# Optimization experiments

Measured on AMD Instinct MI355X. Metric: run time of the kernel, lower is better.

The kernel has to match this reference:

```python
import jax, jax.numpy as jnp
import numpy as np

B, T, C, H = 4, 2048, 768, 12
D = C // H
EPS = 1e-5


def layernorm(x, g, b):
    mu = jnp.mean(x, axis=-1, keepdims=True)
    var = jnp.mean(jnp.square(x - mu), axis=-1, keepdims=True)
    return (x - mu) * jax.lax.rsqrt(var + EPS) * g + b


def setup_inputs() -> dict:
    key = jax.random.key(0)
    ks = jax.random.split(key, 16)
    s = 0.02
    return {
        "x": jax.random.normal(ks[0], (B, T, C), jnp.float32),
        "Wq": jax.random.normal(ks[1], (C, C), jnp.float32) * s,
        "bq": jnp.zeros((C,), jnp.float32),
        "Wk": jax.random.normal(ks[2], (C, C), jnp.float32) * s,
        "bk": jnp.zeros((C,), jnp.float32),
        "Wv": jax.random.normal(ks[3], (C, C), jnp.float32) * s,
        "bv": jnp.zeros((C,), jnp.float32),
        "Wo": jax.random.normal(ks[4], (C, C), jnp.float32) * s,
        "bo": jnp.zeros((C,), jnp.float32),
        "g1": jnp.ones((C,), jnp.float32),
        "b1": jnp.zeros((C,), jnp.float32),
        "g2": jnp.ones((C,), jnp.float32),
        "b2": jnp.zeros((C,), jnp.float32),
        "W1": jax.random.normal(ks[5], (C, 4 * C), jnp.float32) * s,
        "bm1": jnp.zeros((4 * C,), jnp.float32),
        "W2": jax.random.normal(ks[6], (4 * C, C), jnp.float32) * s,
        "bm2": jnp.zeros((C,), jnp.float32),
    }


def reference(x, Wq, bq, Wk, bk, Wv, bv, Wo, bo, g1, b1, g2, b2, W1, bm1, W2, bm2):
    # --- attention branch ---
    h = layernorm(x, g1, b1)
    q = (h @ Wq + bq).reshape(B, T, H, D)
    k = (h @ Wk + bk).reshape(B, T, H, D)
    v = (h @ Wv + bv).reshape(B, T, H, D)
    att = jnp.einsum('bqhd,bkhd->bhqk', q, k) / jnp.sqrt(jnp.float32(D))
    causal = jnp.tril(jnp.ones((T, T), bool))
    att = jnp.where(causal, att, -jnp.inf)
    att = jax.nn.softmax(att, axis=-1)
    o = jnp.einsum('bhqk,bkhd->bqhd', att, v).reshape(B, T, C)
    x = x + o @ Wo + bo
    # --- MLP branch ---
    h = layernorm(x, g2, b2)
    h = jax.nn.gelu(h @ W1 + bm1, approximate=False)
    return x + h @ W2 + bm2
```

## Files before the change

### kernel.cpp

```cpp
#include <hip/hip_runtime.h>
#include <hip/hip_bf16.h>

#define B_ 4
#define T_ 2048
#define C_ 768
#define H_ 12
#define D_ 64
#define QS_ 2304

typedef __attribute__((ext_vector_type(8))) short short8;
typedef __attribute__((ext_vector_type(4))) short short4v;
typedef __attribute__((ext_vector_type(4))) float f32x4;

__device__ __forceinline__ unsigned short f2bf(float f) {
    __hip_bfloat16 h = __float2bfloat16(f);
    return *reinterpret_cast<unsigned short*>(&h);
}

__device__ __forceinline__ unsigned cvt_pk_bf16(float lo, float hi) {
    unsigned r;
    asm("v_cvt_pk_bf16_f32 %0, %1, %2" : "=v"(r) : "v"(lo), "v"(hi));
    return r;
}

__device__ __forceinline__ void gl_lds16(const void* g, void* l) {
    __builtin_amdgcn_global_load_lds((const __attribute__((address_space(1))) unsigned int*)g,
                                     (__attribute__((address_space(3))) unsigned int*)l,
                                     16, 0, 0);
}

__device__ __forceinline__ void transpose_dev(const float* __restrict__ W,
                                              unsigned short* __restrict__ Wt,
                                              int K, int N, int bx, int by,
                                              float (*t)[65]) {
    int n0 = bx * 64, k0 = by * 64;
    int r = threadIdx.x >> 4, c4 = (threadIdx.x & 15) * 4;
    #pragma unroll
    for (int i = 0; i < 4; ++i) {
        float4 v = *(const float4*)(W + (size_t)(k0 + i * 16 + r) * N + n0 + c4);
        t[i*16 + r][c4 + 0] = v.x;
        t[i*16 + r][c4 + 1] = v.y;
        t[i*16 + r][c4 + 2] = v.z;
        t[i*16 + r][c4 + 3] = v.w;
    }
    __syncthreads();
    #pragma unroll
    for (int i = 0; i < 4; ++i) {
        ushort4 o;
        o.x = f2bf(t[c4 + 0][i*16 + r]);
        o.y = f2bf(t[c4 + 1][i*16 + r]);
        o.z = f2bf(t[c4 + 2][i*16 + r]);
        o.w = f2bf(t[c4 + 3][i*16 + r]);
        *(ushort4*)(Wt + (size_t)(n0 + i * 16 + r) * K + k0 + c4) = o;
    }
}

__global__ __launch_bounds__(256) void prep_all(const float* __restrict__ Wq,
                                                const float* __restrict__ Wk,
                                                const float* __restrict__ Wv,
                                                const float* __restrict__ Wo,
                                                const float* __restrict__ W1,
                                                const float* __restrict__ W2,
                                                const float* __restrict__ bq,
                                                const float* __restrict__ bk,
                                                const float* __restrict__ bv,
                                                const float* __restrict__ x,
                                                const float* __restrict__ g1,
                                                const float* __restrict__ b1,
                                                unsigned short* __restrict__ wqkvt,
                                                unsigned short* __restrict__ wot,
                                                unsigned short* __restrict__ w1t,
                                                unsigned short* __restrict__ w2t,
                                                float* __restrict__ bqkv,
                                                unsigned short* __restrict__ ln1h) {
    __shared__ float t[64][65];
    __shared__ float ws[8];
    int blk = blockIdx.x;
    int tid = threadIdx.x;

    if (blk < 576) {
        int which = blk / 144, idx = blk % 144;
        const float* src = (which == 0) ? Wq : (which == 1) ? Wk : (which == 2) ? Wv : Wo;
        unsigned short* dst = (which == 3) ? wot : wqkvt + (size_t)which * C_ * C_;
        transpose_dev(src, dst, C_, C_, idx % 12, idx / 12, t);
    } else if (blk < 1152) {
        int idx = blk - 576;
        transpose_dev(W1, w1t, C_, 4 * C_, idx % 48, idx / 48, t);
    } else if (blk < 1728) {
        int idx = blk - 1152;
        transpose_dev(W2, w2t, 4 * C_, C_, idx % 12, idx / 12, t);
    } else if (blk < 1737) {
        int i = (blk - 1728) * 256 + tid;
        bqkv[i] = (i < 768) ? bq[i] : (i < 1536) ? bk[i - 768] : bv[i - 1536];
    } else {
        int row = blk - 1737;
        const float* xr = x + (size_t)row * C_;
        float v0 = xr[tid], v1 = xr[tid + 256], v2 = xr[tid + 512];
        float s = v0 + v1 + v2;
        #pragma unroll
        for (int off = 1; off < 64; off <<= 1) s += __shfl_xor(s, off);
        int wid = tid >> 6, lane = tid & 63;
        if (lane == 0) ws[wid] = s;
        __syncthreads();
        float mean = (ws[0] + ws[1] + ws[2] + ws[3]) * (1.0f / C_);
        float d0 = v0 - mean, d1 = v1 - mean, d2 = v2 - mean;
        float qs = d0*d0 + d1*d1 + d2*d2;
        #pragma unroll
        for (int off = 1; off < 64; off <<= 1) qs += __shfl_xor(qs, off);
        if (lane == 0) ws[4 + wid] = qs;
        __syncthreads();
        float var = (ws[4] + ws[5] + ws[6] + ws[7]) * (1.0f / C_);
        float rs = rsqrtf(var + 1e-5f);
        unsigned short* orow = ln1h + (size_t)row * C_;
        orow[tid]       = f2bf(d0 * rs * g1[tid]       + b1[tid]);
        orow[tid + 256] = f2bf(d1 * rs * g1[tid + 256] + b1[tid + 256]);
        orow[tid + 512] = f2bf(d2 * rs * g1[tid + 512] + b1[tid + 512]);
    }
}

__global__ __launch_bounds__(256) void ln_f32_bf16(const float* __restrict__ x,
                                                   const float* __restrict__ g,
                                                   const float* __restrict__ b,
                                                   unsigned short* __restrict__ out) {
    int row = blockIdx.x;
    int tid = threadIdx.x;
    const float* xr = x + (size_t)row * C_;
    float v0 = xr[tid], v1 = xr[tid + 256], v2 = xr[tid + 512];
    float s = v0 + v1 + v2;
    #pragma unroll
    for (int off = 1; off < 64; off <<= 1) s += __shfl_xor(s, off);
    __shared__ float ws1[4], ws2[4];
    int wid = tid >> 6, lane = tid & 63;
    if (lane == 0) ws1[wid] = s;
    __syncthreads();
    float mean = (ws1[0] + ws1[1] + ws1[2] + ws1[3]) * (1.0f / C_);
    float d0 = v0 - mean, d1 = v1 - mean, d2 = v2 - mean;
    float qs = d0*d0 + d1*d1 + d2*d2;
    #pragma unroll
    for (int off = 1; off < 64; off <<= 1) qs += __shfl_xor(qs, off);
    if (lane == 0) ws2[wid] = qs;
    __syncthreads();
    float var = (ws2[0] + ws2[1] + ws2[2] + ws2[3]) * (1.0f / C_);
    float rs = rsqrtf(var + 1e-5f);
    unsigned short* orow = out + (size_t)row * C_;
    orow[tid]       = f2bf(d0 * rs * g[tid]       + b[tid]);
    orow[tid + 256] = f2bf(d1 * rs * g[tid + 256] + b[tid + 256]);
    orow[tid + 512] = f2bf(d2 * rs * g[tid + 512] + b[tid + 512]);
}

template <int EPI>
__global__ __launch_bounds__(256) void gemm_bf16(const unsigned short* __restrict__ A,
                                                 const unsigned short* __restrict__ Bt,
                                                 const float* __restrict__ bias,
                                                 const float* __restrict__ resid,
                                                 void* __restrict__ Cout,
                                                 unsigned short* __restrict__ aux,
                                                 int M, int N, int K, int gx) {
    __shared__ short As[2][128 * 32];
    __shared__ short Bs[2][128 * 32];
    int tid = threadIdx.x;
    int w = tid >> 6, l = tid & 63;
    int nb = gridDim.x;
    int per = nb >> 3;
    int fid = (int)blockIdx.x;
    int wid = (fid & 7) * per + (fid >> 3);
    int bn = wid % gx, bm = wid / gx;
    int wr = w >> 1, wc = w & 1;

    f32x4 acc[4][4];
    #pragma unroll
    for (int m = 0; m < 4; ++m)
        #pragma unroll
        for (int n = 0; n < 4; ++n)
            acc[m][n] = (f32x4){0.f, 0.f, 0.f, 0.f};

    const short* Ag = (const short*)A + (size_t)(bm * 128) * K;
    const short* Bg = (const short*)Bt + (size_t)(bn * 128) * K;
    int srow = tid >> 2;
    int scol = (tid & 3) * 8;
    int lrow = l & 15, lk = (l >> 4) * 8;

    auto stage = [&](int buf, int k0) {
        #pragma unroll
        for (int i = 0; i < 2; ++i) {
            gl_lds16(Ag + (size_t)(i * 64 + srow) * K + k0 + scol,
                     (char*)&As[buf][0] + i * 4096 + w * 1024);
            gl_lds16(Bg + (size_t)(i * 64 + srow) * K + k0 + scol,
                     (char*)&Bs[buf][0] + i * 4096 + w * 1024);
        }
    };

    int nk = K / 32;
    stage(0, 0);
    __syncthreads();

    for (int kt = 0; kt < nk; ++kt) {
        int cur = kt & 1;
        if (kt + 1 < nk) stage(cur ^ 1, (kt + 1) * 32);

        short8 av[4], bv[4];
        #pragma unroll
        for (int m = 0; m < 4; ++m)
            av[m] = *(const short8*)&As[cur][(wr * 64 + m * 16 + lrow) * 32 + lk];
        #pragma unroll
        for (int n = 0; n < 4; ++n)
            bv[n] = *(const short8*)&Bs[cur][(wc * 64 + n * 16 + lrow) * 32 + lk];
        #pragma unroll
        for (int m = 0; m < 4; ++m)
            #pragma unroll
            for (int n = 0; n < 4; ++n)
                acc[m][n] = __builtin_amdgcn_mfma_f32_16x16x32_bf16(av[m], bv[n], acc[m][n], 0, 0, 0);

        __syncthreads();
    }

    int lcol = l & 15, lr4 = (l >> 4) * 4;
    int row0 = bm * 128 + wr * 64;
    int col0 = bn * 128 + wc * 64;
    #pragma unroll
    for (int m = 0; m < 4; ++m) {
        #pragma unroll
        for (int n = 0; n < 4; ++n) {
            int col = col0 + n * 16 + lcol;
            float bz = bias[col];
            if (EPI == 5 && col0 >= 1536) {
                ushort4 o4;
                o4.x = f2bf(acc[m][n][0] + bz);
                o4.y = f2bf(acc[m][n][1] + bz);
                o4.z = f2bf(acc[m][n][2] + bz);
                o4.w = f2bf(acc[m][n][3] + bz);
                int row = row0 + m * 16 + lr4;
                int c = col - 1536;
                *(ushort4*)(aux + ((size_t)(row >> 11) * 768 + c) * (size_t)T_ + (row & 2047)) = o4;
            } else {
                #pragma unroll
                for (int r = 0; r < 4; ++r) {
                    int row = row0 + m * 16 + lr4 + r;
                    float v = acc[m][n][r] + bz;
                    if (EPI == 1) {
                        float u = fmaf(0.044715f * v, v * v, v);
                        float e = __builtin_amdgcn_exp2f(u * -2.3022127f);
                        v = v * __builtin_amdgcn_rcpf(1.0f + e);
                        ((unsigned short*)Cout)[(size_t)row * N + col] = f2bf(v);
                    } else if (EPI == 2) {
                        v += resid[(size_t)row * N + col];
                        ((float*)Cout)[(size_t)row * N + col] = v;
                    } else {
                        ((unsigned short*)Cout)[(size_t)row * N + col] = f2bf(v);
                    }
                }
            }
        }
    }
}

__global__ __launch_bounds__(256) void attn_v9(const unsigned short* __restrict__ QKV,
                                               const unsigned short* __restrict__ vT,
                                               unsigned short* __restrict__ O) {
    __shared__ short Ks[128 * 64];
    __shared__ short Vt[64 * 128];

    int tid = threadIdx.x;
    int w = tid >> 6, l = tid & 63;
    int g = l >> 4, lc = l & 15;
    int wid = (int)(blockIdx.x & 7) * 192 + (int)(blockIdx.x >> 3);
    int bh = wid >> 5;
    int a  = 31 - (wid & 31);
    int b = bh / H_, h = bh % H_;
    const size_t bT = (size_t)b * T_;
    const unsigned short* Qp = QKV + h * D_;
    const unsigned short* Kp = QKV + 768 + h * D_;
    const unsigned short* vTb = vT + ((size_t)b * 768 + h * 64) * (size_t)T_;
    const float SCL = 0.125f * 1.44269504088896340736f;

    int qw = a * 64 + w * 16;

    short8 qf[2];
    {
        const unsigned short* qp = Qp + (bT + qw + lc) * QS_;
        qf[0] = *(const short8*)(qp + g * 8);
        qf[1] = *(const short8*)(qp + 32 + g * 8);
    }

    f32x4 oacc[4];
    #pragma unroll
    for (int n = 0; n < 4; ++n) oacc[n] = (f32x4){0.f, 0.f, 0.f, 0.f};
    float mrun = 4.0f, lpart = 0.f;

    int ntiles = (a >> 1) + 1;
    for (int kt = 0; kt < ntiles; ++kt) {
        int k0 = kt * 128;
        if (kt) __syncthreads();

        #pragma unroll
        for (int c = 0; c < 4; ++c) {
            int row = w * 32 + c * 8 + (l >> 3);
            int inner = (l & 7) * 16;
            const char* src = (const char*)(Kp + (bT + k0 + row) * QS_)
                              + (inner ^ ((row & 7) << 4));
            gl_lds16(src, (char*)Ks + w * 4096 + c * 1024);
        }
        #pragma unroll
        for (int c = 0; c < 4; ++c) {
            int d = w * 16 + c * 4 + (l >> 4);
            int inner = (l & 15) * 16;
            const char* src = (const char*)(vTb + (size_t)d * T_ + k0)
                              + (inner ^ ((d & 7) << 4));
            gl_lds16(src, (char*)Vt + w * 4096 + c * 1024);
        }
        __syncthreads();

        uint2 qd[8];
        float lmaxP[4] = {-INFINITY, -INFINITY, -INFINITY, -INFINITY};
        float rsumP[4] = {0.f, 0.f, 0.f, 0.f};
        bool full = (k0 + 127 <= qw);
        #pragma unroll
        for (int mk = 0; mk < 8; ++mk) {
            f32x4 s = (f32x4){0.f, 0.f, 0.f, 0.f};
            __builtin_amdgcn_s_setprio(1);
            #pragma unroll
            for (int ksd = 0; ksd < 2; ++ksd) {
                int row = mk * 16 + lc;
                int byt = (row * 128 + ksd * 64 + g * 16) ^ ((row & 7) << 4);
                short8 av = *(const short8*)((char*)Ks + byt);
                s = __builtin_amdgcn_mfma_f32_16x16x32_bf16(av, qf[ksd], s, 0, 0, 0);
            }
            __builtin_amdgcn_s_setprio(0);
            float p[4];
            #pragma unroll
            for (int r = 0; r < 4; ++r) {
                float sv = s[r] * SCL;
                if (!full && (k0 + mk * 16 + g * 4 + r > qw + lc)) sv = -INFINITY;
                lmaxP[r] = fmaxf(lmaxP[r], sv);
                float pv = __builtin_amdgcn_exp2f(sv - mrun);
                p[r] = pv;
                rsumP[r] += pv;
            }
            qd[mk].x = cvt_pk_bf16(p[0], p[1]);
            qd[mk].y = cvt_pk_bf16(p[2], p[3]);
        }
        float lmax = fmaxf(fmaxf(lmaxP[0], lmaxP[1]), fmaxf(lmaxP[2], lmaxP[3]));
        lpart += (rsumP[0] + rsumP[1]) + (rsumP[2] + rsumP[3]);

        #pragma unroll
        for (int ks = 0; ks < 4; ++ks) {
            uint2 qa = qd[ks * 2], qb = qd[ks * 2 + 1];
            int srcLo = lc + ((g & 1) << 5);
            int srcHi = srcLo + 16;
            unsigned a0 = (unsigned)__shfl((int)qa.x, srcLo);
            unsigned a1 = (unsigned)__shfl((int)qa.y, srcLo);
            unsigned a2 = (unsigned)__shfl((int)qa.x, srcHi);
            unsigned a3 = (unsigned)__shfl((int)qa.y, srcHi);
            unsigned b0 = (unsigned)__shfl((int)qb.x, srcLo);
            unsigned b1 = (unsigned)__shfl((int)qb.y, srcLo);
            unsigned b2 = (unsigned)__shfl((int)qb.x, srcHi);
            unsigned b3 = (unsigned)__shfl((int)qb.y, srcHi);
            bool lo = (g < 2);
            union { unsigned u[4]; short8 s8; } pa;
            pa.u[0] = lo ? a0 : b0;
            pa.u[1] = lo ? a1 : b1;
            pa.u[2] = lo ? a2 : b2;
            pa.u[3] = lo ? a3 : b3;
            short8 vbv[4];
            #pragma unroll
            for (int n = 0; n < 4; ++n) {
                int row = n * 16 + lc;
                int byt = (row * 256 + ks * 64 + g * 16) ^ ((row & 7) << 4);
                vbv[n] = *(const short8*)((char*)Vt + byt);
            }
            __builtin_amdgcn_s_setprio(1);
            #pragma unroll
            for (int n = 0; n < 4; ++n)
                oacc[n] = __builtin_amdgcn_mfma_f32_16x16x32_bf16(pa.s8, vbv[n], oacc[n], 0, 0, 0);
            __builtin_amdgcn_s_setprio(0);
        }

        if (__any(lmax > mrun + 8.0f)) {
            lmax = fmaxf(lmax, __shfl_xor(lmax, 16));
            lmax = fmaxf(lmax, __shfl_xor(lmax, 32));
            float mnew = fmaxf(mrun, lmax);
            float cc = __builtin_amdgcn_exp2f(mrun - mnew);
            lpart *= cc;
            mrun = mnew;
            #pragma unroll
            for (int r = 0; r < 4; ++r) {
                float cr = __shfl(cc, (l & 48) + g * 4 + r);
                #pragma unroll
                for (int n = 0; n < 4; ++n) oacc[n][r] *= cr;
            }
        }
    }

    float lv = lpart;
    lv += __shfl_xor(lv, 16);
    lv += __shfl_xor(lv, 32);
    float linv = 1.0f / lv;
    float inv[4];
    #pragma unroll
    for (int r = 0; r < 4; ++r) inv[r] = __shfl(linv, (l & 48) + g * 4 + r);
    #pragma unroll
    for (int n = 0; n < 4; ++n) {
        int col = h * D_ + n * 16 + lc;
        #pragma unroll
        for (int r = 0; r < 4; ++r) {
            int row = qw + g * 4 + r;
            O[(bT + row) * C_ + col] = f2bf(oacc[n][r] * inv[r]);
        }
    }
}

extern "C" void kernel_launch(void* const* d_in, const int* in_sizes, int n_in,
                              void* d_out, int out_size, void* d_ws, size_t ws_size,
                              hipStream_t stream) {
    const float* x   = (const float*)d_in[0];
    const float* Wq  = (const float*)d_in[1];
    const float* bq  = (const float*)d_in[2];
    const float* Wk  = (const float*)d_in[3];
    const float* bk  = (const float*)d_in[4];
    const float* Wv  = (const float*)d_in[5];
    const float* bv  = (const float*)d_in[6];
    const float* Wo  = (const float*)d_in[7];
    const float* bo  = (const float*)d_in[8];
    const float* g1  = (const float*)d_in[9];
    const float* b1  = (const float*)d_in[10];
    const float* g2  = (const float*)d_in[11];
    const float* b2  = (const float*)d_in[12];
    const float* W1  = (const float*)d_in[13];
    const float* bm1 = (const float*)d_in[14];
    const float* W2  = (const float*)d_in[15];
    const float* bm2 = (const float*)d_in[16];
    float* out = (float*)d_out;

    const size_t S = (size_t)B_ * T_ * C_;
    char* base = (char*)d_ws;
    unsigned short* ln1h = (unsigned short*)base;
    unsigned short* qkvb = (unsigned short*)(base + 2 * S);
    unsigned short* o    = ln1h;
    unsigned short* ln2h = qkvb;
    unsigned short* vT   = (unsigned short*)(base + 8 * S);
    unsigned short* hid  = (unsigned short*)(base + 4 * S);
    float* xmid          = (float*)(base + 12 * S);
    unsigned short* wqkvt = (unsigned short*)(base + 16 * S);
    unsigned short* wot   = wqkvt + (size_t)3 * C_ * C_;
    unsigned short* w1t   = wot + (size_t)C_ * C_;
    unsigned short* w2t   = w1t + (size_t)C_ * 4 * C_;
    float* bqkv           = (float*)(w2t + (size_t)C_ * 4 * C_);

    const int M = B_ * T_;
    dim3 blk(256);

    prep_all<<<dim3(1737 + M), blk, 0, stream>>>(Wq, Wk, Wv, Wo, W1, W2,
                                                 bq, bk, bv, x, g1, b1,
                                                 wqkvt, wot, w1t, w2t, bqkv, ln1h);

    gemm_bf16<5><<<dim3((QS_ / 128) * (M / 128)), blk, 0, stream>>>(ln1h, wqkvt, bqkv, nullptr, qkvb, vT, M, QS_, C_, QS_ / 128);

    attn_v9<<<dim3(B_ * H_ * 32), blk, 0, stream>>>(qkvb, vT, o);

    gemm_bf16<2><<<dim3((C_ / 128) * (M / 128)), blk, 0, stream>>>(o, wot, bo, x, xmid, nullptr, M, C_, C_, C_ / 128);
    ln_f32_bf16<<<dim3(M), blk, 0, stream>>>(xmid, g2, b2, ln2h);
    gemm_bf16<1><<<dim3((4 * C_ / 128) * (M / 128)), blk, 0, stream>>>(ln2h, w1t, bm1, nullptr, hid, nullptr, M, 4 * C_, C_, 4 * C_ / 128);
    gemm_bf16<2><<<dim3((C_ / 128) * (M / 128)), blk, 0, stream>>>(hid, w2t, bm2, xmid, out, nullptr, M, C_, 4 * C_, C_ / 128);
}
```

Baseline: 298.9 us.

## Compute transposed PV product with 16x16x16 MFMA to drop P shuffles

The attention PV step now computes O^T = V^T P^T using the 16x16x16 bf16 MFMA. The P fragment produced by the QK^T MFMA can then be used directly as the B operand, with no cross-lane shuffles or selects. Because the output is transposed, each lane holds one query row. The rescale therefore needs no per-row shuffle, and the final store becomes a vectorized 4-element write. The cost is twice as many MFMA instructions of half the K depth, plus narrower 8-byte LDS reads of V.

```diff
diff --git a/kernel.cpp b/kernel.cpp
--- a/kernel.cpp
+++ b/kernel.cpp
@@ -27,6 +27,21 @@
     __builtin_amdgcn_global_load_lds((const __attribute__((address_space(1))) unsigned int*)g,
                                      (__attribute__((address_space(3))) unsigned int*)l,
                                      16, 0, 0);
+}
+
+#if defined(__has_builtin)
+#if __has_builtin(__builtin_amdgcn_mfma_f32_16x16x16bf16_1k)
+#define HAVE_MFMA16 1
+#endif
+#endif
+
+__device__ __forceinline__ f32x4 mfma16(short4v a, short4v b, f32x4 c) {
+#ifdef HAVE_MFMA16
+    return __builtin_amdgcn_mfma_f32_16x16x16bf16_1k(a, b, c, 0, 0, 0);
+#else
+    asm("v_mfma_f32_16x16x16_bf16 %0, %1, %2, %0" : "+v"(c) : "v"(a), "v"(b));
+    return c;
+#endif
 }
 
 __device__ __forceinline__ void transpose_dev(const float* __restrict__ W,
@@ -254,9 +269,9 @@
     }
 }
 
-__global__ __launch_bounds__(256) void attn_v9(const unsigned short* __restrict__ QKV,
-                                               const unsigned short* __restrict__ vT,
-                                               unsigned short* __restrict__ O) {
+__global__ __launch_bounds__(256) void attn_v10(const unsigned short* __restrict__ QKV,
+                                                const unsigned short* __restrict__ vT,
+                                                unsigned short* __restrict__ O) {
     __shared__ short Ks[128 * 64];
     __shared__ short Vt[64 * 128];
 
@@ -282,9 +297,9 @@
         qf[1] = *(const short8*)(qp + 32 + g * 8);
     }
 
-    f32x4 oacc[4];
-    #pragma unroll
-    for (int n = 0; n < 4; ++n) oacc[n] = (f32x4){0.f, 0.f, 0.f, 0.f};
+    f32x4 oaccT[4];
+    #pragma unroll
+    for (int n = 0; n < 4; ++n) oaccT[n] = (f32x4){0.f, 0.f, 0.f, 0.f};
     float mrun = 4.0f, lpart = 0.f;
 
     int ntiles = (a >> 1) + 1;
@@ -343,35 +358,20 @@
         lpart += (rsumP[0] + rsumP[1]) + (rsumP[2] + rsumP[3]);
 
         #pragma unroll
-        for (int ks = 0; ks < 4; ++ks) {
-            uint2 qa = qd[ks * 2], qb = qd[ks * 2 + 1];
-            int srcLo = lc + ((g & 1) << 5);
-            int srcHi = srcLo + 16;
-            unsigned a0 = (unsigned)__shfl((int)qa.x, srcLo);
-            unsigned a1 = (unsigned)__shfl((int)qa.y, srcLo);
-            unsigned a2 = (unsigned)__shfl((int)qa.x, srcHi);
-            unsigned a3 = (unsigned)__shfl((int)qa.y, srcHi);
-            unsigned b0 = (unsigned)__shfl((int)qb.x, srcLo);
-            unsigned b1 = (unsigned)__shfl((int)qb.y, srcLo);
-            unsigned b2 = (unsigned)__shfl((int)qb.x, srcHi);
-            unsigned b3 = (unsigned)__shfl((int)qb.y, srcHi);
-            bool lo = (g < 2);
-            union { unsigned u[4]; short8 s8; } pa;
-            pa.u[0] = lo ? a0 : b0;
-            pa.u[1] = lo ? a1 : b1;
-            pa.u[2] = lo ? a2 : b2;
-            pa.u[3] = lo ? a3 : b3;
-            short8 vbv[4];
+        for (int mk = 0; mk < 8; ++mk) {
+            union { uint2 u2; short4v s4; } pb;
+            pb.u2 = qd[mk];
+            short4v va[4];
             #pragma unroll
             for (int n = 0; n < 4; ++n) {
-                int row = n * 16 + lc;
-                int byt = (row * 256 + ks * 64 + g * 16) ^ ((row & 7) << 4);
-                vbv[n] = *(const short8*)((char*)Vt + byt);
+                int d = n * 16 + lc;
+                int byt = (d * 256 + mk * 32 + g * 8) ^ ((d & 7) << 4);
+                va[n] = *(const short4v*)((char*)Vt + byt);
             }
             __builtin_amdgcn_s_setprio(1);
             #pragma unroll
             for (int n = 0; n < 4; ++n)
-                oacc[n] = __builtin_amdgcn_mfma_f32_16x16x32_bf16(pa.s8, vbv[n], oacc[n], 0, 0, 0);
+                oaccT[n] = mfma16(va[n], pb.s4, oaccT[n]);
             __builtin_amdgcn_s_setprio(0);
         }
 
@@ -383,10 +383,9 @@
             lpart *= cc;
             mrun = mnew;
             #pragma unroll
-            for (int r = 0; r < 4; ++r) {
-                float cr = __shfl(cc, (l & 48) + g * 4 + r);
-                #pragma unroll
-                for (int n = 0; n < 4; ++n) oacc[n][r] *= cr;
+            for (int n = 0; n < 4; ++n) {
+                oaccT[n][0] *= cc; oaccT[n][1] *= cc;
+                oaccT[n][2] *= cc; oaccT[n][3] *= cc;
             }
         }
     }
@@ -394,18 +393,16 @@
     float lv = lpart;
     lv += __shfl_xor(lv, 16);
     lv += __shfl_xor(lv, 32);
-    float linv = 1.0f / lv;
-    float inv[4];
-    #pragma unroll
-    for (int r = 0; r < 4; ++r) inv[r] = __shfl(linv, (l & 48) + g * 4 + r);
+    float inv = 1.0f / lv;
+    unsigned short* orow = O + (bT + qw + lc) * C_ + h * D_;
     #pragma unroll
     for (int n = 0; n < 4; ++n) {
-        int col = h * D_ + n * 16 + lc;
-        #pragma unroll
-        for (int r = 0; r < 4; ++r) {
-            int row = qw + g * 4 + r;
-            O[(bT + row) * C_ + col] = f2bf(oacc[n][r] * inv[r]);
-        }
+        ushort4 o4;
+        o4.x = f2bf(oaccT[n][0] * inv);
+        o4.y = f2bf(oaccT[n][1] * inv);
+        o4.z = f2bf(oaccT[n][2] * inv);
+        o4.w = f2bf(oaccT[n][3] * inv);
+        *(ushort4*)(orow + n * 16 + g * 4) = o4;
     }
 }
 
@@ -455,7 +452,7 @@
 
     gemm_bf16<5><<<dim3((QS_ / 128) * (M / 128)), blk, 0, stream>>>(ln1h, wqkvt, bqkv, nullptr, qkvb, vT, M, QS_, C_, QS_ / 128);
 
-    attn_v9<<<dim3(B_ * H_ * 32), blk, 0, stream>>>(qkvb, vT, o);
+    attn_v10<<<dim3(B_ * H_ * 32), blk, 0, stream>>>(qkvb, vT, o);
 
     gemm_bf16<2><<<dim3((C_ / 128) * (M / 128)), blk, 0, stream>>>(o, wot, bo, x, xmid, nullptr, M, C_, C_, C_ / 128);
     ln_f32_bf16<<<dim3(M), blk, 0, stream>>>(xmid, g2, b2, ln2h);
```

New measurement: 301.2 us. About the same (+0.8%).
